# Optimization experiments

Hardware: AMD Instinct MI355X
Metric: run time of the kernel (lower is better)

## Reference

```python
import jax, jax.numpy as jnp
import numpy as np

B, C, Ci, V = 1024, 256, 128, 90
EPS = 1e-5


def setup_inputs() -> dict:
    key = jax.random.key(0)
    ks = iter(jax.random.split(key, 40))
    def nrm(shape, s=1.0):
        return jax.random.normal(next(ks), shape, jnp.float32) * s
    def uni(shape):
        return jax.random.uniform(next(ks), shape, jnp.float32, 0.5, 1.5)
    inp = {"x1": nrm((B, C, V)), "x2": nrm((B, C, V))}
    for p in ["g", "th", "ph"]:
        inp[p + "_bn_gamma"] = uni((C,))
        inp[p + "_bn_beta"] = nrm((C,), 0.1)
        inp[p + "_bn_mean"] = nrm((C,), 0.1)
        inp[p + "_bn_var"] = uni((C,))
        inp[p + "_w"] = nrm((Ci, C), 0.05)
        inp[p + "_b"] = nrm((Ci,), 0.05)
    inp["W_w"] = nrm((C, Ci), 0.05)
    inp["W_b"] = nrm((C,), 0.05)
    inp["W_bn_gamma"] = uni((C,))
    inp["W_bn_beta"] = nrm((C,), 0.1)
    inp["W_bn_mean"] = nrm((C,), 0.1)
    inp["W_bn_var"] = uni((C,))
    inp["qt_w"] = nrm((Ci, C), 0.05); inp["qt_b"] = nrm((Ci,), 0.05)
    inp["ks_w"] = nrm((Ci, V), 0.05); inp["ks_b"] = nrm((Ci,), 0.05)
    inp["qs_w"] = nrm((Ci, V), 0.05); inp["qs_b"] = nrm((Ci,), 0.05)
    inp["kt_w"] = nrm((Ci, C), 0.05); inp["kt_b"] = nrm((Ci,), 0.05)
    return inp


def _bn(x, g, b, m, v):
    # eval-mode BatchNorm1d over channel dim of (B, C, V)
    return (x - m[:, None]) * jax.lax.rsqrt(v[:, None] + EPS) * g[:, None] + b[:, None]


def _conv1(x, w, b):
    # 1x1 Conv1d: (B, Cin, V) x (Cout, Cin) -> (B, Cout, V)
    return jnp.einsum('bcv,oc->bov', x, w) + b[:, None]


def reference(x1, x2,
              g_bn_gamma, g_bn_beta, g_bn_mean, g_bn_var, g_w, g_b,
              th_bn_gamma, th_bn_beta, th_bn_mean, th_bn_var, th_w, th_b,
              ph_bn_gamma, ph_bn_beta, ph_bn_mean, ph_bn_var, ph_w, ph_b,
              W_w, W_b, W_bn_gamma, W_bn_beta, W_bn_mean, W_bn_var,
              qt_w, qt_b, ks_w, ks_b, qs_w, qs_b, kt_w, kt_b):
    g_x1 = _conv1(_bn(x1, g_bn_gamma, g_bn_beta, g_bn_mean, g_bn_var), g_w, g_b)
    g_x2 = _conv1(_bn(x2, g_bn_gamma, g_bn_beta, g_bn_mean, g_bn_var), g_w, g_b)
    theta = _conv1(_bn(x1, th_bn_gamma, th_bn_beta, th_bn_mean, th_bn_var), th_w, th_b)  # theta(x1)
    phi = _conv1(_bn(x2, ph_bn_gamma, ph_bn_beta, ph_bn_mean, ph_bn_var), ph_w, ph_b)    # phi(x2)

    e_time = jnp.einsum('biv,bjv->bij', theta, phi)   # (B, Ci, Ci) = theta_x1 @ phi_x2
    e_space = jnp.einsum('bci,bcj->bij', theta, phi)  # (B, V, V)  = theta_x2 @ phi_x1

    attn_time_1 = jax.nn.softmax(e_time, axis=-1)
    attn_time_2 = jax.nn.softmax(jnp.swapaxes(e_time, 1, 2), axis=-1)
    attn_space_2 = jax.nn.softmax(e_space, axis=-1)
    attn_space_1 = jax.nn.softmax(jnp.swapaxes(e_space, 1, 2), axis=-1)

    z1 = jnp.einsum('bij,bjv,bvw->biw', attn_time_2, g_x1, attn_space_2)  # (B, Ci, V)
    z2 = jnp.einsum('bij,bjv,bvw->biw', attn_time_1, g_x2, attn_space_1)

    m1t = x1.mean(axis=2)                      # (B, C)
    q_time = m1t @ qt_w.T + qt_b               # (B, Ci)
    k_space = x2.mean(axis=1) @ ks_w.T + ks_b  # (B, Ci)
    # bmm of (B,1,Ci) x (B,Ci,1) -> (B,1,1); softmax over singleton dim == 1 (kept for faithfulness)
    attn_t2s = jax.nn.softmax(jnp.sum(q_time * k_space, axis=-1, keepdims=True)[:, :, None], axis=-1)
    x2n = x2 + attn_t2s * m1t[:, :, None]      # broadcast (B,1,1)*(B,C,1) over V

    q_space = x1.mean(axis=1) @ qs_w.T + qs_b  # (B, Ci)
    k_time = x2n.mean(axis=2) @ kt_w.T + kt_b  # (B, Ci)
    attn_s2t = jax.nn.softmax(jnp.sum(q_space * k_time, axis=-1, keepdims=True)[:, :, None], axis=-1)
    x1n = x1 + attn_s2t * x2n.mean(axis=1)[:, None, :]

    def Wop(z):
        return _bn(_conv1(z, W_w, W_b), W_bn_gamma, W_bn_beta, W_bn_mean, W_bn_var)

    return (x1n + Wop(z1), x2n + Wop(z2))
```

## Files before the change

kernel.cpp:

```cpp
#include <hip/hip_runtime.h>

namespace {

constexpr int B = 1024;

using u16 = unsigned short;
using u32 = unsigned int;

typedef __attribute__((ext_vector_type(8))) short bf16x8;
typedef __attribute__((ext_vector_type(4))) float f32x4;

#define MFMA16(a, b, c) __builtin_amdgcn_mfma_f32_16x16x32_bf16(a, b, c, 0, 0, 0)

__device__ __forceinline__ u16 f2bf(float f) {
  u32 u = __builtin_bit_cast(u32, f);
  u += 0x7FFFu + ((u >> 16) & 1u);
  return (u16)(u >> 16);
}
__device__ __forceinline__ float bf2f(u16 s) {
  u32 u = ((u32)s) << 16;
  return __builtin_bit_cast(float, u);
}
__device__ __forceinline__ u32 packbf2(float a, float b) {
  return (u32)f2bf(a) | ((u32)f2bf(b) << 16);
}
__device__ __forceinline__ u32 tsplit(float f) {
  u32 u = __builtin_bit_cast(u32, f);
  float r = f - __builtin_bit_cast(float, u & 0xFFFF0000u);
  u32 ur = __builtin_bit_cast(u32, r);
  return (u >> 16) | (ur & 0xFFFF0000u);
}

__global__ __launch_bounds__(256) void k0_fold(
    const float* __restrict__ gg, const float* __restrict__ gbe, const float* __restrict__ gme, const float* __restrict__ gva,
    const float* __restrict__ gw, const float* __restrict__ gbi,
    const float* __restrict__ tg, const float* __restrict__ tbe, const float* __restrict__ tme, const float* __restrict__ tva,
    const float* __restrict__ tw, const float* __restrict__ tbi,
    const float* __restrict__ pg, const float* __restrict__ pbe, const float* __restrict__ pme, const float* __restrict__ pva,
    const float* __restrict__ pw, const float* __restrict__ pbi,
    const float* __restrict__ Ww, const float* __restrict__ Wb,
    const float* __restrict__ Wg2, const float* __restrict__ Wbe, const float* __restrict__ Wme, const float* __restrict__ Wva,
    u16* __restrict__ wgo, float* __restrict__ bgo,
    u16* __restrict__ wthi, u16* __restrict__ wtlo, float* __restrict__ bto,
    u16* __restrict__ wphi, u16* __restrict__ wplo, float* __restrict__ bpo,
    u16* __restrict__ wWo, float* __restrict__ bWo)
{
  __shared__ float red[4];
  const int blk = blockIdx.x, tid = threadIdx.x;
  if (blk < 384) {
    const int p = blk >> 7, o = blk & 127;
    const float *ga, *be, *me, *va, *wm, *bi;
    if (p == 0)      { ga = gg; be = gbe; me = gme; va = gva; wm = gw; bi = gbi; }
    else if (p == 1) { ga = tg; be = tbe; me = tme; va = tva; wm = tw; bi = tbi; }
    else             { ga = pg; be = pbe; me = pme; va = pva; wm = pw; bi = pbi; }
    float s = ga[tid] * rsqrtf(va[tid] + 1e-5f);
    float t = be[tid] - me[tid] * s;
    float wv = wm[o * 256 + tid];
    float val = wv * s;
    if (p == 0) {
      wgo[o * 256 + tid] = f2bf(val);
    } else {
      u16 hi = f2bf(val);
      u16 lo = f2bf(val - bf2f(hi));
      if (p == 1) { wthi[o * 256 + tid] = hi; wtlo[o * 256 + tid] = lo; }
      else        { wphi[o * 256 + tid] = hi; wplo[o * 256 + tid] = lo; }
    }
    float part = t * wv;
#pragma unroll
    for (int off = 32; off; off >>= 1) part += __shfl_down(part, off);
    if ((tid & 63) == 0) red[tid >> 6] = part;
    __syncthreads();
    if (tid == 0) {
      float bsum = bi[o] + red[0] + red[1] + red[2] + red[3];
      if (p == 0) bgo[o] = bsum; else if (p == 1) bto[o] = bsum; else bpo[o] = bsum;
    }
  } else {
    const int c = blk - 384;
    float sW = Wg2[c] * rsqrtf(Wva[c] + 1e-5f);
    if (tid < 128) wWo[c * 128 + tid] = f2bf(Ww[c * 128 + tid] * sW);
    if (tid == 0) bWo[c] = Wb[c] * sW + Wbe[c] - Wme[c] * sW;
  }
}

__global__ __launch_bounds__(512, 4) void k1_conv(
    const float* __restrict__ x1, const float* __restrict__ x2,
    const u16* __restrict__ wG, const float* __restrict__ bG,
    const u16* __restrict__ wTh, const u16* __restrict__ wTl, const float* __restrict__ bT,
    const u16* __restrict__ wPh, const u16* __restrict__ wPl, const float* __restrict__ bP,
    u32* __restrict__ thRm, u32* __restrict__ phRm,
    u16* __restrict__ outU,
    float* __restrict__ m1t, float* __restrict__ x2cm, float* __restrict__ x1am)
{
  __shared__ u32 qb[64 * 92];
  __shared__ u16 xh[96 * 136];
  __shared__ u16 xl[96 * 136];
  __shared__ float red[4];
  const int b = blockIdx.x, tid = threadIdx.x;
  const int l = tid & 63, wv = tid >> 6, lr = l & 15, lq = l >> 4;
  const f32x4 zero = {0.f, 0.f, 0.f, 0.f};

  auto doPhase = [&](const float* __restrict__ xb,
                     const u16* __restrict__ Wh, const u16* __restrict__ Wl, const float* __restrict__ biasT,
                     u32* __restrict__ rmDst, u32* __restrict__ pkDst, u16* __restrict__ gDst, bool isX1) {
    f32x4 aT[6], aG[6];
#pragma unroll
    for (int i = 0; i < 6; ++i) { aT[i] = zero; aG[i] = zero; }
    float cs = 0.f;
    for (int h = 0; h < 2; ++h) {
      for (int q = 0; q < 2; ++q) {
        __syncthreads();
        const float* src = xb + (2 * h + q) * 5760;
        for (int t = tid; t < 2880; t += 512) {
          float2 f = *(const float2*)(src + 2 * t);
          int cl = (2 * t) / 90, v = 2 * t - 90 * cl;
          uint2 w; w.x = tsplit(f.x); w.y = tsplit(f.y);
          *(uint2*)&qb[cl * 92 + v] = w;
        }
        __syncthreads();
        for (int t = tid; t < 1440; t += 512) {
          int v = t % 90, c4 = t / 90;
          u32 p0 = qb[(4 * c4 + 0) * 92 + v], p1 = qb[(4 * c4 + 1) * 92 + v];
          u32 p2 = qb[(4 * c4 + 2) * 92 + v], p3 = qb[(4 * c4 + 3) * 92 + v];
          uint2 hi, lo;
          hi.x = (p0 & 0xFFFFu) | (p1 << 16);
          hi.y = (p2 & 0xFFFFu) | (p3 << 16);
          lo.x = (p0 >> 16) | (p1 & 0xFFFF0000u);
          lo.y = (p2 >> 16) | (p3 & 0xFFFF0000u);
          int base = v * 136 + 64 * q + 4 * c4;
          *(uint2*)&xh[base] = hi;
          *(uint2*)&xl[base] = lo;
        }
        if (q == 1) {
          for (int t = tid; t < 384; t += 512) {
            int v = 90 + (t >> 6), c2 = (t & 63) * 2;
            *(u32*)&xh[v * 136 + c2] = 0u;
            *(u32*)&xl[v * 136 + c2] = 0u;
          }
        }
        if (!isX1 && tid < 90) {
          float s = 0.f;
          for (int cl = 0; cl < 64; ++cl) {
            u32 p = qb[cl * 92 + tid];
            s += bf2f((u16)p) + bf2f((u16)(p >> 16));
          }
          cs += s;
        }
      }
      __syncthreads();
      if (isX1 && tid < 128) {
        float s = 0.f;
        for (int v = 0; v < 90; ++v) s += bf2f(xh[v * 136 + tid]) + bf2f(xl[v * 136 + tid]);
        m1t[b * 256 + 128 * h + tid] = s * (1.f / 90.f);
#pragma unroll
        for (int o = 32; o; o >>= 1) s += __shfl_down(s, o);
        if ((tid & 63) == 0) red[(tid >> 6) + 2 * h] = s;
      }
      for (int kk = 0; kk < 4; ++kk) {
        const int wo = (16 * wv + lr) * 256 + 128 * h + kk * 32 + 8 * lq;
        bf16x8 ah = *(const bf16x8*)(Wh + wo);
        bf16x8 al = *(const bf16x8*)(Wl + wo);
        bf16x8 ag = *(const bf16x8*)(wG + wo);
#pragma unroll
        for (int nt = 0; nt < 6; ++nt) {
          const int bo = (16 * nt + lr) * 136 + kk * 32 + 8 * lq;
          bf16x8 bh = *(const bf16x8*)&xh[bo];
          bf16x8 bl = *(const bf16x8*)&xl[bo];
          aT[nt] = MFMA16(ah, bh, aT[nt]);
          aT[nt] = MFMA16(ah, bl, aT[nt]);
          aT[nt] = MFMA16(al, bh, aT[nt]);
          aG[nt] = MFMA16(ag, bh, aG[nt]);
        }
      }
    }
    __syncthreads();
    const int c0 = 16 * wv + 4 * lq;
    const float4 bt4 = *(const float4*)(biasT + c0);
    const float4 bg4 = *(const float4*)(bG + c0);
#pragma unroll
    for (int nt = 0; nt < 6; ++nt) {
      const int v = 16 * nt + lr;
      u32 pk0, pk1, pk2, pk3; uint2 gpk;
      if (v < 90) {
        pk0 = tsplit(aT[nt][0] + bt4.x);
        pk1 = tsplit(aT[nt][1] + bt4.y);
        pk2 = tsplit(aT[nt][2] + bt4.z);
        pk3 = tsplit(aT[nt][3] + bt4.w);
        gpk.x = packbf2(aG[nt][0] + bg4.x, aG[nt][1] + bg4.y);
        gpk.y = packbf2(aG[nt][2] + bg4.z, aG[nt][3] + bg4.w);
      } else { pk0 = pk1 = pk2 = pk3 = 0u; gpk.x = 0u; gpk.y = 0u; }
      uint4 q4; q4.x = pk0; q4.y = pk1; q4.z = pk2; q4.w = pk3;
      *(uint4*)(pkDst + v * 128 + c0) = q4;
      rmDst[(c0 + 0) * 96 + v] = pk0;
      rmDst[(c0 + 1) * 96 + v] = pk1;
      rmDst[(c0 + 2) * 96 + v] = pk2;
      rmDst[(c0 + 3) * 96 + v] = pk3;
      *(uint2*)(gDst + v * 128 + c0) = gpk;
    }
    if (isX1) {
      if (tid == 0) x1am[b] = (red[0] + red[1] + red[2] + red[3]) * (1.f / 23040.f);
    } else {
      if (tid < 90) x2cm[b * 96 + tid] = cs * (1.f / 256.f);
    }
  };

  u16* o1 = outU + (size_t)b * 46080;
  u16* o2 = outU + (size_t)(1024 + b) * 46080;
  doPhase(x1 + (size_t)b * 23040, wTh, wTl, bT,
          thRm + (size_t)b * 12288, (u32*)(o1 + 12288), o1, true);
  doPhase(x2 + (size_t)b * 23040, wPh, wPl, bP,
          phRm + (size_t)b * 12288, (u32*)(o2 + 12288), o2, false);
}

__global__ __launch_bounds__(512) void k2_attn(
    const u32* __restrict__ thRm, const u32* __restrict__ phRm,
    u16* __restrict__ outU,
    u16* __restrict__ At1g, u16* __restrict__ At2g)
{
  __shared__ __align__(16) char smem[108544];
  u16* s0 = (u16*)smem;
  float* st = (float*)(smem + 106496);
  float* eL = (float*)smem;

  const int b = blockIdx.x, tid = threadIdx.x;
  const int l = tid & 63, wv = tid >> 6, lr = l & 15, lq = l >> 4;
  const f32x4 zero = {0.f, 0.f, 0.f, 0.f};

  const u32* thRmB = thRm + (size_t)b * 12288;
  const u32* phRmB = phRm + (size_t)b * 12288;
  const u32* thPk = (const u32*)(outU + (size_t)b * 46080 + 12288);
  const u32* phPk = (const u32*)(outU + (size_t)(1024 + b) * 46080 + 12288);
  u32* S1 = (u32*)(outU + (size_t)(1024 + b) * 46080 + 36864);
  u32* S2 = (u32*)(outU + (size_t)b * 46080 + 36864);

  u16* th_hi = s0;
  u16* th_lo = s0 + 13312;
  u16* ph_hi = s0 + 26624;
  u16* ph_lo = s0 + 39936;
  for (int d = tid; d < 6144; d += 512) {
    int ten = (d >= 3072);
    int i = d - 3072 * ten;
    int ci = i / 24, q4 = i - 24 * ci;
    uint4 P = *(const uint4*)((ten ? phRmB : thRmB) + ci * 96 + 4 * q4);
    uint2 hi, lo;
    hi.x = (P.x & 0xFFFFu) | (P.y << 16);
    hi.y = (P.z & 0xFFFFu) | (P.w << 16);
    lo.x = (P.x >> 16) | (P.y & 0xFFFF0000u);
    lo.y = (P.z >> 16) | (P.w & 0xFFFF0000u);
    *(uint2*)((ten ? ph_hi : th_hi) + ci * 104 + 4 * q4) = hi;
    *(uint2*)((ten ? ph_lo : th_lo) + ci * 104 + 4 * q4) = lo;
  }
  __syncthreads();
  f32x4 acc[8];
#pragma unroll
  for (int nt = 0; nt < 8; ++nt) acc[nt] = zero;
#pragma unroll
  for (int kk = 0; kk < 3; ++kk) {
    const int ao = (16 * wv + lr) * 104 + kk * 32 + 8 * lq;
    bf16x8 ah = *(const bf16x8*)&th_hi[ao];
    bf16x8 al = *(const bf16x8*)&th_lo[ao];
#pragma unroll
    for (int nt = 0; nt < 8; ++nt) {
      const int bo = (16 * nt + lr) * 104 + kk * 32 + 8 * lq;
      bf16x8 bh = *(const bf16x8*)&ph_hi[bo];
      bf16x8 bl = *(const bf16x8*)&ph_lo[bo];
      acc[nt] = MFMA16(ah, bh, acc[nt]);
      acc[nt] = MFMA16(ah, bl, acc[nt]);
      acc[nt] = MFMA16(al, bh, acc[nt]);
    }
  }
  __syncthreads();
#pragma unroll
  for (int nt = 0; nt < 8; ++nt)
#pragma unroll
    for (int r = 0; r < 4; ++r)
      eL[(16 * nt + lr) * 133 + 16 * wv + 4 * lq + r] = acc[nt][r];
  __syncthreads();
  if (tid < 128) {
    int j = tid; float m = -1e30f;
    for (int i = 0; i < 128; ++i) m = fmaxf(m, eL[j * 133 + i]);
    float s = 0.f;
    for (int i = 0; i < 128; ++i) s += __expf(eL[j * 133 + i] - m);
    st[j] = m; st[128 + j] = 1.f / s;
  } else if (tid < 256) {
    int i = tid - 128; float m = -1e30f;
    for (int j = 0; j < 128; ++j) m = fmaxf(m, eL[j * 133 + i]);
    float s = 0.f;
    for (int j = 0; j < 128; ++j) s += __expf(eL[j * 133 + i] - m);
    st[256 + i] = m; st[384 + i] = 1.f / s;
  }
  __syncthreads();
  {
    u32* A1 = (u32*)(At1g + (size_t)b * 16384);
    u32* A2 = (u32*)(At2g + (size_t)b * 16384);
    for (int d = tid; d < 8192; d += 512) {
      int i = d >> 6, jp = d & 63;
      float m1 = st[256 + i], s1v = st[384 + i];
      float a0 = __expf(eL[(2 * jp) * 133 + i] - m1) * s1v;
      float a1 = __expf(eL[(2 * jp + 1) * 133 + i] - m1) * s1v;
      A1[d] = packbf2(a0, a1);
      float m2 = st[i], s2v = st[128 + i];
      float b0 = __expf(eL[i * 133 + 2 * jp] - m2) * s2v;
      float b1 = __expf(eL[i * 133 + 2 * jp + 1] - m2) * s2v;
      A2[d] = packbf2(b0, b1);
    }
  }
  __syncthreads();

  u16* tTh = s0;
  u16* tTl = s0 + 13056;
  u16* pTh = s0 + 26112;
  u16* pTl = s0 + 39168;
  for (int d = tid; d < 6144; d += 512) {
    int ten = (d >= 3072);
    int i = d - 3072 * ten;
    int v = i >> 5, q4 = i & 31;
    uint4 P = *(const uint4*)((ten ? phPk : thPk) + v * 128 + 4 * q4);
    uint2 hi, lo;
    hi.x = (P.x & 0xFFFFu) | (P.y << 16);
    hi.y = (P.z & 0xFFFFu) | (P.w << 16);
    lo.x = (P.x >> 16) | (P.y & 0xFFFF0000u);
    lo.y = (P.z >> 16) | (P.w & 0xFFFF0000u);
    *(uint2*)((ten ? pTh : tTh) + v * 136 + 4 * q4) = hi;
    *(uint2*)((ten ? pTl : tTl) + v * 136 + 4 * q4) = lo;
  }
  __syncthreads();
  f32x4 accS[5];
#pragma unroll
  for (int it = 0; it < 5; ++it) accS[it] = zero;
#pragma unroll
  for (int it = 0; it < 5; ++it) {
    const int t5 = wv + 8 * it;
    if (t5 < 36) {
      const int mt = t5 / 6, nt = t5 - 6 * (t5 / 6);
#pragma unroll
      for (int kk = 0; kk < 4; ++kk) {
        const int ao = (16 * mt + lr) * 136 + kk * 32 + 8 * lq;
        const int bo = (16 * nt + lr) * 136 + kk * 32 + 8 * lq;
        bf16x8 ah = *(const bf16x8*)&tTh[ao];
        bf16x8 al = *(const bf16x8*)&tTl[ao];
        bf16x8 bh = *(const bf16x8*)&pTh[bo];
        bf16x8 bl = *(const bf16x8*)&pTl[bo];
        accS[it] = MFMA16(ah, bh, accS[it]);
        accS[it] = MFMA16(ah, bl, accS[it]);
        accS[it] = MFMA16(al, bh, accS[it]);
      }
    }
  }
  __syncthreads();
  {
    float* esL = (float*)smem;
#pragma unroll
    for (int it = 0; it < 5; ++it) {
      const int t5 = wv + 8 * it;
      if (t5 < 36) {
        const int mt = t5 / 6, nt = t5 - 6 * (t5 / 6);
#pragma unroll
        for (int r = 0; r < 4; ++r)
          esL[(16 * nt + lr) * 101 + 16 * mt + 4 * lq + r] = accS[it][r];
      }
    }
  }
  __syncthreads();
  {
    float* esL = (float*)smem;
    if (tid < 96) {
      int v = tid; float m = -1e30f;
      for (int w2 = 0; w2 < 90; ++w2) m = fmaxf(m, esL[v * 101 + w2]);
      float s = 0.f;
      for (int w2 = 0; w2 < 90; ++w2) s += __expf(esL[v * 101 + w2] - m);
      st[v] = m; st[128 + v] = 1.f / s;
    } else if (tid >= 128 && tid < 224) {
      int v = tid - 128; float m = -1e30f;
      for (int w2 = 0; w2 < 90; ++w2) m = fmaxf(m, esL[w2 * 101 + v]);
      float s = 0.f;
      for (int w2 = 0; w2 < 90; ++w2) s += __expf(esL[w2 * 101 + v] - m);
      st[256 + v] = m; st[384 + v] = 1.f / s;
    }
  }
  __syncthreads();
  {
    float* esL = (float*)smem;
    for (int d = tid; d < 4608; d += 512) {
      int w2 = d / 48, vp = d - 48 * (d / 48);
      int v0 = 2 * vp, v1 = v0 + 1;
      float a0 = __expf(esL[v0 * 101 + w2] - st[v0]) * st[128 + v0];
      float a1 = __expf(esL[v1 * 101 + w2] - st[v1]) * st[128 + v1];
      S1[d] = packbf2(a0, a1);
      float b0 = __expf(esL[w2 * 101 + v0] - st[256 + v0]) * st[384 + v0];
      float b1 = __expf(esL[w2 * 101 + v1] - st[256 + v1]) * st[384 + v1];
      S2[d] = packbf2(b0, b1);
    }
  }
}

__global__ __launch_bounds__(256) void k3_out(
    const float* __restrict__ x1, const float* __restrict__ x2,
    const u16* __restrict__ At1g, const u16* __restrict__ At2g,
    const u16* __restrict__ wW, const float* __restrict__ bW,
    const float* __restrict__ m1t, const float* __restrict__ x2cm, const float* __restrict__ x1am,
    float* __restrict__ out)
{
  __shared__ __align__(16) char smem[53248];
  u16* gT = (u16*)smem;
  u16* ZT = (u16*)smem;
  u16* Tb = (u16*)(smem + 26624);
  const int b = blockIdx.x, tid = threadIdx.x;
  const int l = tid & 63, wv = tid >> 6, lr = l & 15, lq = l >> 4;
  const f32x4 zero = {0.f, 0.f, 0.f, 0.f};

  float* out1 = out + (size_t)b * 23040;
  float* out2 = out + (size_t)23040 * 1024 + (size_t)b * 23040;
  const u16* g1s = (const u16*)out1;
  const u16* g2s = (const u16*)out2;
  const u16* As1 = (const u16*)out2 + 36864;
  const u16* As2 = (const u16*)out1 + 36864;

  auto phase = [&](const u16* __restrict__ gsrc, const u16* __restrict__ At,
                   const u16* __restrict__ AsT, const float* __restrict__ xres,
                   float* __restrict__ dst, bool modeA) {
    for (int i = tid; i < 1536; i += 256) {
      int v = i >> 4, hh = i & 15;
      *(uint4*)&gT[v * 136 + 8 * hh] = ((const uint4*)gsrc)[i];
    }
    __syncthreads();
#pragma unroll
    for (int ni = 0; ni < 2; ++ni) {
      const int nt = 2 * wv + ni;
      f32x4 acc[6];
#pragma unroll
      for (int i = 0; i < 6; ++i) acc[i] = zero;
#pragma unroll
      for (int kk = 0; kk < 4; ++kk) {
        bf16x8 bb = *(const bf16x8*)(At + (16 * nt + lr) * 128 + kk * 32 + 8 * lq);
#pragma unroll
        for (int mt = 0; mt < 6; ++mt) {
          bf16x8 a = *(const bf16x8*)&gT[(16 * mt + lr) * 136 + kk * 32 + 8 * lq];
          acc[mt] = MFMA16(a, bb, acc[mt]);
        }
      }
#pragma unroll
      for (int mt = 0; mt < 6; ++mt) {
        uint2 pk;
        pk.x = packbf2(acc[mt][0], acc[mt][1]);
        pk.y = packbf2(acc[mt][2], acc[mt][3]);
        *(uint2*)&Tb[(16 * nt + lr) * 104 + 16 * mt + 4 * lq] = pk;
      }
    }
    __syncthreads();
    {
      f32x4 acc[2][6];
#pragma unroll
      for (int i = 0; i < 2; ++i)
#pragma unroll
        for (int j = 0; j < 6; ++j) acc[i][j] = zero;
#pragma unroll
      for (int kk = 0; kk < 3; ++kk) {
        bf16x8 a0 = *(const bf16x8*)&Tb[(16 * (2 * wv) + lr) * 104 + kk * 32 + 8 * lq];
        bf16x8 a1 = *(const bf16x8*)&Tb[(16 * (2 * wv + 1) + lr) * 104 + kk * 32 + 8 * lq];
#pragma unroll
        for (int nt = 0; nt < 6; ++nt) {
          bf16x8 bb = *(const bf16x8*)(AsT + (16 * nt + lr) * 96 + kk * 32 + 8 * lq);
          acc[0][nt] = MFMA16(a0, bb, acc[0][nt]);
          acc[1][nt] = MFMA16(a1, bb, acc[1][nt]);
        }
      }
#pragma unroll
      for (int mi = 0; mi < 2; ++mi) {
        const int mt = 2 * wv + mi;
#pragma unroll
        for (int nt = 0; nt < 6; ++nt) {
          uint2 pk;
          pk.x = packbf2(acc[mi][nt][0], acc[mi][nt][1]);
          pk.y = packbf2(acc[mi][nt][2], acc[mi][nt][3]);
          *(uint2*)&ZT[(16 * nt + lr) * 136 + 16 * mt + 4 * lq] = pk;
        }
      }
    }
    __syncthreads();
    const float am = modeA ? 0.f : x1am[b];
#pragma unroll
    for (int mi = 0; mi < 4; ++mi) {
      const int mt = 4 * wv + mi;
      f32x4 acc[6];
#pragma unroll
      for (int i = 0; i < 6; ++i) acc[i] = zero;
#pragma unroll
      for (int kk = 0; kk < 4; ++kk) {
        bf16x8 a = *(const bf16x8*)(wW + (16 * mt + lr) * 128 + kk * 32 + 8 * lq);
#pragma unroll
        for (int nt = 0; nt < 6; ++nt) {
          bf16x8 bb = *(const bf16x8*)&ZT[(16 * nt + lr) * 136 + kk * 32 + 8 * lq];
          acc[nt] = MFMA16(a, bb, acc[nt]);
        }
      }
      const int c0 = 16 * mt + 4 * lq;
      const float4 bw4 = *(const float4*)(bW + c0);
      float bwA[4] = {bw4.x, bw4.y, bw4.z, bw4.w};
      float mA[4] = {0.f, 0.f, 0.f, 0.f};
      if (modeA) {
        const float4 m4 = *(const float4*)(m1t + b * 256 + c0);
        mA[0] = m4.x; mA[1] = m4.y; mA[2] = m4.z; mA[3] = m4.w;
      }
#pragma unroll
      for (int nt = 0; nt < 6; ++nt) {
        const int v = 16 * nt + lr;
        if (v < 90) {
          const float addv = modeA ? 0.f : (am + x2cm[b * 96 + v]);
#pragma unroll
          for (int r = 0; r < 4; ++r) {
            const int c = c0 + r;
            const float extra = modeA ? mA[r] : addv;
            dst[c * 90 + v] = xres[c * 90 + v] + acc[nt][r] + bwA[r] + extra;
          }
        }
      }
    }
    __syncthreads();
  };

  phase(g2s, At1g + (size_t)b * 16384, As1, x2 + (size_t)b * 23040, out2, true);
  phase(g1s, At2g + (size_t)b * 16384, As2, x1 + (size_t)b * 23040, out1, false);
}

}

extern "C" void kernel_launch(void* const* d_in, const int* in_sizes, int n_in,
                              void* d_out, int out_size, void* d_ws, size_t ws_size,
                              hipStream_t stream)
{
  (void)in_sizes; (void)n_in; (void)out_size; (void)ws_size;
  const float* x1  = (const float*)d_in[0];
  const float* x2  = (const float*)d_in[1];
  const float* gg  = (const float*)d_in[2];
  const float* gbe = (const float*)d_in[3];
  const float* gme = (const float*)d_in[4];
  const float* gva = (const float*)d_in[5];
  const float* gw  = (const float*)d_in[6];
  const float* gbi = (const float*)d_in[7];
  const float* tg  = (const float*)d_in[8];
  const float* tbe = (const float*)d_in[9];
  const float* tme = (const float*)d_in[10];
  const float* tva = (const float*)d_in[11];
  const float* tw  = (const float*)d_in[12];
  const float* tbi = (const float*)d_in[13];
  const float* pg  = (const float*)d_in[14];
  const float* pbe = (const float*)d_in[15];
  const float* pme = (const float*)d_in[16];
  const float* pva = (const float*)d_in[17];
  const float* pw  = (const float*)d_in[18];
  const float* pbi = (const float*)d_in[19];
  const float* Ww  = (const float*)d_in[20];
  const float* Wb  = (const float*)d_in[21];
  const float* Wg  = (const float*)d_in[22];
  const float* Wbe = (const float*)d_in[23];
  const float* Wme = (const float*)d_in[24];
  const float* Wva = (const float*)d_in[25];

  float* out = (float*)d_out;
  unsigned char* W8 = (unsigned char*)d_ws;

  size_t off = 0;
  auto al = [&](size_t n) { size_t r = off; off += (n + 255) & ~(size_t)255; return r; };
  const size_t oWG  = al(65536);
  const size_t oWTh = al(65536), oWTl = al(65536);
  const size_t oWPh = al(65536), oWPl = al(65536);
  const size_t oWW  = al(65536);
  const size_t oBG = al(512), oBT = al(512), oBP = al(512), oBW = al(1024);
  const size_t oRM1 = al((size_t)B * 49152), oRM2 = al((size_t)B * 49152);
  const size_t oA1 = al((size_t)B * 32768), oA2 = al((size_t)B * 32768);
  const size_t oM1 = al((size_t)B * 1024), oXC = al((size_t)B * 384), oXA = al((size_t)B * 4);

  k0_fold<<<dim3(640), dim3(256), 0, stream>>>(
      gg, gbe, gme, gva, gw, gbi,
      tg, tbe, tme, tva, tw, tbi,
      pg, pbe, pme, pva, pw, pbi,
      Ww, Wb, Wg, Wbe, Wme, Wva,
      (u16*)(W8 + oWG), (float*)(W8 + oBG),
      (u16*)(W8 + oWTh), (u16*)(W8 + oWTl), (float*)(W8 + oBT),
      (u16*)(W8 + oWPh), (u16*)(W8 + oWPl), (float*)(W8 + oBP),
      (u16*)(W8 + oWW), (float*)(W8 + oBW));

  k1_conv<<<dim3(B), dim3(512), 0, stream>>>(
      x1, x2,
      (const u16*)(W8 + oWG), (const float*)(W8 + oBG),
      (const u16*)(W8 + oWTh), (const u16*)(W8 + oWTl), (const float*)(W8 + oBT),
      (const u16*)(W8 + oWPh), (const u16*)(W8 + oWPl), (const float*)(W8 + oBP),
      (u32*)(W8 + oRM1), (u32*)(W8 + oRM2),
      (u16*)out,
      (float*)(W8 + oM1), (float*)(W8 + oXC), (float*)(W8 + oXA));

  k2_attn<<<dim3(B), dim3(512), 0, stream>>>(
      (const u32*)(W8 + oRM1), (const u32*)(W8 + oRM2),
      (u16*)out,
      (u16*)(W8 + oA1), (u16*)(W8 + oA2));

  k3_out<<<dim3(B), dim3(256), 0, stream>>>(
      x1, x2,
      (const u16*)(W8 + oA1), (const u16*)(W8 + oA2),
      (const u16*)(W8 + oWW), (const float*)(W8 + oBW),
      (const float*)(W8 + oM1), (const float*)(W8 + oXC), (const float*)(W8 + oXA),
      out);
}
```

Before: 500.6 us.

## Drop transposed hi/lo LDS buffers and build MFMA operands from packed staging

```diff
diff --git a/kernel.cpp b/kernel.cpp
--- a/kernel.cpp
+++ b/kernel.cpp
@@ -82,7 +82,7 @@
   }
 }
 
-__global__ __launch_bounds__(512, 4) void k1_conv(
+__global__ __launch_bounds__(512, 6) void k1_conv(
     const float* __restrict__ x1, const float* __restrict__ x2,
     const u16* __restrict__ wG, const float* __restrict__ bG,
     const u16* __restrict__ wTh, const u16* __restrict__ wTl, const float* __restrict__ bT,
@@ -91,13 +91,16 @@
     u16* __restrict__ outU,
     float* __restrict__ m1t, float* __restrict__ x2cm, float* __restrict__ x1am)
 {
-  __shared__ u32 qb[64 * 92];
-  __shared__ u16 xh[96 * 136];
-  __shared__ u16 xl[96 * 136];
-  __shared__ float red[4];
+  __shared__ u32 qb[128 * 97];
+  __shared__ float red[8];
   const int b = blockIdx.x, tid = threadIdx.x;
   const int l = tid & 63, wv = tid >> 6, lr = l & 15, lq = l >> 4;
   const f32x4 zero = {0.f, 0.f, 0.f, 0.f};
+
+  for (int t = tid; t < 128 * 6; t += 512) {
+    int c = t / 6, v = 90 + t % 6;
+    qb[c * 97 + v] = 0u;
+  }
 
   auto doPhase = [&](const float* __restrict__ xb,
                      const u16* __restrict__ Wh, const u16* __restrict__ Wl, const float* __restrict__ biasT,
@@ -107,64 +110,60 @@
     for (int i = 0; i < 6; ++i) { aT[i] = zero; aG[i] = zero; }
     float cs = 0.f;
     for (int h = 0; h < 2; ++h) {
-      for (int q = 0; q < 2; ++q) {
-        __syncthreads();
-        const float* src = xb + (2 * h + q) * 5760;
-        for (int t = tid; t < 2880; t += 512) {
-          float2 f = *(const float2*)(src + 2 * t);
-          int cl = (2 * t) / 90, v = 2 * t - 90 * cl;
-          uint2 w; w.x = tsplit(f.x); w.y = tsplit(f.y);
-          *(uint2*)&qb[cl * 92 + v] = w;
-        }
-        __syncthreads();
-        for (int t = tid; t < 1440; t += 512) {
-          int v = t % 90, c4 = t / 90;
-          u32 p0 = qb[(4 * c4 + 0) * 92 + v], p1 = qb[(4 * c4 + 1) * 92 + v];
-          u32 p2 = qb[(4 * c4 + 2) * 92 + v], p3 = qb[(4 * c4 + 3) * 92 + v];
-          uint2 hi, lo;
-          hi.x = (p0 & 0xFFFFu) | (p1 << 16);
-          hi.y = (p2 & 0xFFFFu) | (p3 << 16);
-          lo.x = (p0 >> 16) | (p1 & 0xFFFF0000u);
-          lo.y = (p2 >> 16) | (p3 & 0xFFFF0000u);
-          int base = v * 136 + 64 * q + 4 * c4;
-          *(uint2*)&xh[base] = hi;
-          *(uint2*)&xl[base] = lo;
-        }
-        if (q == 1) {
-          for (int t = tid; t < 384; t += 512) {
-            int v = 90 + (t >> 6), c2 = (t & 63) * 2;
-            *(u32*)&xh[v * 136 + c2] = 0u;
-            *(u32*)&xl[v * 136 + c2] = 0u;
+      __syncthreads();
+      const float* src = xb + h * 11520;
+      for (int t = tid; t < 5760; t += 512) {
+        float2 f = *(const float2*)(src + 2 * t);
+        int e = 2 * t, c = e / 90, v = e - 90 * c;
+        qb[c * 97 + v]     = tsplit(f.x);
+        qb[c * 97 + v + 1] = tsplit(f.y);
+      }
+      __syncthreads();
+      if (isX1) {
+        if (tid < 128) {
+          float s = 0.f;
+          for (int v = 0; v < 90; ++v) {
+            u32 p = qb[tid * 97 + v];
+            s += bf2f((u16)p) + bf2f((u16)(p >> 16));
           }
-        }
-        if (!isX1 && tid < 90) {
+          m1t[b * 256 + 128 * h + tid] = s * (1.f / 90.f);
+#pragma unroll
+          for (int o = 32; o; o >>= 1) s += __shfl_down(s, o);
+          if ((tid & 63) == 0) red[(tid >> 6) + 2 * h] = s;
+        }
+      } else {
+        if (tid < 90) {
           float s = 0.f;
-          for (int cl = 0; cl < 64; ++cl) {
-            u32 p = qb[cl * 92 + tid];
+          for (int c = 0; c < 128; ++c) {
+            u32 p = qb[c * 97 + tid];
             s += bf2f((u16)p) + bf2f((u16)(p >> 16));
           }
           cs += s;
         }
-      }
-      __syncthreads();
-      if (isX1 && tid < 128) {
-        float s = 0.f;
-        for (int v = 0; v < 90; ++v) s += bf2f(xh[v * 136 + tid]) + bf2f(xl[v * 136 + tid]);
-        m1t[b * 256 + 128 * h + tid] = s * (1.f / 90.f);
-#pragma unroll
-        for (int o = 32; o; o >>= 1) s += __shfl_down(s, o);
-        if ((tid & 63) == 0) red[(tid >> 6) + 2 * h] = s;
       }
       for (int kk = 0; kk < 4; ++kk) {
         const int wo = (16 * wv + lr) * 256 + 128 * h + kk * 32 + 8 * lq;
         bf16x8 ah = *(const bf16x8*)(Wh + wo);
         bf16x8 al = *(const bf16x8*)(Wl + wo);
         bf16x8 ag = *(const bf16x8*)(wG + wo);
+        const int c0 = kk * 32 + 8 * lq;
 #pragma unroll
         for (int nt = 0; nt < 6; ++nt) {
-          const int bo = (16 * nt + lr) * 136 + kk * 32 + 8 * lq;
-          bf16x8 bh = *(const bf16x8*)&xh[bo];
-          bf16x8 bl = *(const bf16x8*)&xl[bo];
+          const int v = 16 * nt + lr;
+          const u32* qp = qb + c0 * 97 + v;
+          u32 w0 = qp[0], w1 = qp[97], w2 = qp[194], w3 = qp[291];
+          u32 w4 = qp[388], w5 = qp[485], w6 = qp[582], w7 = qp[679];
+          uint4 hh, ll;
+          hh.x = (w0 & 0xFFFFu) | (w1 << 16);
+          hh.y = (w2 & 0xFFFFu) | (w3 << 16);
+          hh.z = (w4 & 0xFFFFu) | (w5 << 16);
+          hh.w = (w6 & 0xFFFFu) | (w7 << 16);
+          ll.x = (w0 >> 16) | (w1 & 0xFFFF0000u);
+          ll.y = (w2 >> 16) | (w3 & 0xFFFF0000u);
+          ll.z = (w4 >> 16) | (w5 & 0xFFFF0000u);
+          ll.w = (w6 >> 16) | (w7 & 0xFFFF0000u);
+          bf16x8 bh = __builtin_bit_cast(bf16x8, hh);
+          bf16x8 bl = __builtin_bit_cast(bf16x8, ll);
           aT[nt] = MFMA16(ah, bh, aT[nt]);
           aT[nt] = MFMA16(ah, bl, aT[nt]);
           aT[nt] = MFMA16(al, bh, aT[nt]);
```

New measurement: 818.3 us. +63.5%, slower.
